# Kernel optimization log

Measured on AMD Instinct MI355X. Metric: run time of the kernel, lower is better.

## Reference

```python
import jax, jax.numpy as jnp
import numpy as np

N, B, T, F_IN, H1, H2 = 69, 32, 1024, 8, 32, 16


def cal_adj_norm(adj):
    # adj_norm = D^-1/2 (A + I) D^-1/2
    n = adj.shape[0]
    adj_ = adj + jnp.eye(n, dtype=adj.dtype)
    d = jnp.sum(adj_, axis=1)
    d_is = d ** -0.5
    return adj_ * d_is[:, None] * d_is[None, :]


def setup_inputs() -> dict:
    key = jax.random.key(0)
    k1, k2, k3, k4 = jax.random.split(key, 4)
    x = jax.random.normal(k1, (N, B, T, F_IN), dtype=jnp.float32)
    a = jax.random.uniform(k2, (N, N), dtype=jnp.float32)
    adj = ((a + a.T) > 1.4).astype(jnp.float32)
    W1 = jax.random.normal(k3, (F_IN, H1), dtype=jnp.float32)
    W2 = jax.random.normal(k4, (H1, H2), dtype=jnp.float32)
    return {"x": x, "adj": adj, "W1": W1, "W2": W2}


def reference(x, adj, W1, W2):
    adj_n = cal_adj_norm(adj)                      # [N, N]
    xb = jnp.transpose(x, (1, 2, 0, 3))            # [B, T, N, F_in]
    # layer 1: relu( adj_n @ x @ W1 ), batched over (B, T)
    h = jax.nn.relu(jnp.einsum('nm,btmf->btnf', adj_n, xb) @ W1)   # [B, T, N, H1]
    # layer 2: sigmoid( adj_n @ h @ W2 )
    out = jax.nn.sigmoid(jnp.einsum('nm,btmf->btnf', adj_n, h) @ W2)  # [B, T, N, H2]
    return out
```

## Files before the change

### kernel.cpp

```cpp
#include <hip/hip_runtime.h>
#include <math.h>

#define N_NODES 69
#define MP      80
#define KP      96
#define BT_TOTAL 32768
#define F_IN    8
#define H1      32
#define H2      16

#define TBT     8
#define BLOCK   256

#define ZPITCH  136
#define HBPITCH 40
#define RSTRIDE 72
#define RROWS   576

typedef __attribute__((ext_vector_type(8))) short bf16x8;
typedef __attribute__((ext_vector_type(4))) float f32x4;

__device__ __forceinline__ unsigned short f2bf(float f) {
    unsigned u = __float_as_uint(f);
    return (unsigned short)((u + 0x7FFFu + ((u >> 16) & 1u)) >> 16);
}
__device__ __forceinline__ float bf2f(unsigned short h) {
    return __uint_as_float(((unsigned)h) << 16);
}

__global__ void setup_kernel(const float* __restrict__ adj,
                             const float* __restrict__ W1,
                             const float* __restrict__ W2,
                             unsigned short* __restrict__ adjh,
                             unsigned short* __restrict__ adjl,
                             unsigned short* __restrict__ W1p,
                             unsigned short* __restrict__ W2p)
{
    __shared__ float dinv[N_NODES];
    const int tid = threadIdx.x;
    if (tid < N_NODES) {
        float s = 1.0f;
        for (int j = 0; j < N_NODES; ++j) s += adj[tid * N_NODES + j];
        dinv[tid] = rsqrtf(s);
    }
    __syncthreads();
    for (int idx = tid; idx < MP * KP; idx += BLOCK) {
        const int n = idx / KP, m = idx % KP;
        float v = 0.0f;
        if (n < N_NODES && m < N_NODES) {
            float a = adj[n * N_NODES + m] + (n == m ? 1.0f : 0.0f);
            v = a * dinv[n] * dinv[m];
        }
        unsigned short h = f2bf(v);
        adjh[idx] = h;
        adjl[idx] = f2bf(v - bf2f(h));
    }
    for (int i = tid; i < 2 * 64 * F_IN; i += BLOCK) {
        const int nt = i >> 9;
        const int ln = (i >> 3) & 63;
        const int j  = i & 7;
        const int q = ln >> 4, l = ln & 15;
        float v = (q == 0) ? W1[j * H1 + nt * 16 + l] : 0.0f;
        W1p[i] = f2bf(v);
    }
    for (int i = tid; i < 64 * F_IN; i += BLOCK) {
        const int ln = i >> 3, j = i & 7;
        const int q = ln >> 4, l = ln & 15;
        W2p[i] = f2bf(W2[(q * 8 + j) * H2 + l]);
    }
}

__global__ __launch_bounds__(BLOCK, 4) void gcn_kernel(
    const float* __restrict__ x,
    const unsigned short* __restrict__ adjh,
    const unsigned short* __restrict__ adjl,
    const unsigned short* __restrict__ W1p,
    const unsigned short* __restrict__ W2p,
    float* __restrict__ out)
{
    __shared__ unsigned short U_s[KP * ZPITCH];
    __shared__ unsigned short Y1_s[RROWS * F_IN];
    __shared__ unsigned short Hb_s[4][16 * HBPITCH];

    const int tid  = threadIdx.x;
    const int lane = tid & 63;
    const int wv   = tid >> 6;
    const int quad = lane >> 4;
    const int l16  = lane & 15;
    const int bt0  = blockIdx.x * TBT;

    for (int i = tid; i < 27 * 64; i += BLOCK) {
        const int row = N_NODES + (i >> 6), w = i & 63;
        ((unsigned*)U_s)[row * 68 + w] = 0u;
    }

    const int btg = bt0 + wv * 2 + (l16 >> 3);
    const int fl  = l16 & 7;

    f32x4 acc[5] = {};
#pragma unroll
    for (int kt = 0; kt < 3; ++kt) {
        union AF { unsigned u[4]; bf16x8 v; } ah, al;
#pragma unroll
        for (int p = 0; p < 4; ++p) {
            const int m0 = kt * 32 + quad * 8 + 2 * p;
            const int m1 = m0 + 1;
            float x0 = 0.0f, x1 = 0.0f;
            if (kt < 2) {
                x0 = x[(size_t)m0 * 262144 + btg * 8 + fl];
                x1 = x[(size_t)m1 * 262144 + btg * 8 + fl];
            } else {
                if (m0 < N_NODES) x0 = x[(size_t)m0 * 262144 + btg * 8 + fl];
                if (m1 < N_NODES) x1 = x[(size_t)m1 * 262144 + btg * 8 + fl];
            }
            const unsigned short h0 = f2bf(x0), h1 = f2bf(x1);
            ah.u[p] = (unsigned)h0 | ((unsigned)h1 << 16);
            const unsigned short g0 = f2bf(x0 - bf2f(h0));
            const unsigned short g1 = f2bf(x1 - bf2f(h1));
            al.u[p] = (unsigned)g0 | ((unsigned)g1 << 16);
        }
#pragma unroll
        for (int nt = 0; nt < 5; ++nt) {
            const int boff = (nt * 16 + l16) * KP + kt * 32 + quad * 8;
            const bf16x8 bh = *(const bf16x8*)(adjh + boff);
            const bf16x8 bl = *(const bf16x8*)(adjl + boff);
            acc[nt] = __builtin_amdgcn_mfma_f32_16x16x32_bf16(ah.v, bh, acc[nt], 0, 0, 0);
            acc[nt] = __builtin_amdgcn_mfma_f32_16x16x32_bf16(ah.v, bl, acc[nt], 0, 0, 0);
            acc[nt] = __builtin_amdgcn_mfma_f32_16x16x32_bf16(al.v, bh, acc[nt], 0, 0, 0);
        }
    }

    {
        const int btc = wv * 2 + (quad >> 1);
        const int fcb = (quad & 1) * 4;
#pragma unroll
        for (int nt = 0; nt < 5; ++nt) {
            const int n = nt * 16 + l16;
            if (n < RSTRIDE) {
#pragma unroll
                for (int reg = 0; reg < 4; ++reg)
                    Y1_s[(btc * RSTRIDE + n) * F_IN + fcb + reg] = f2bf(acc[nt][reg]);
            }
        }
    }

    const bf16x8 w1f0 = *(const bf16x8*)&W1p[lane * 8];
    const bf16x8 w1f1 = *(const bf16x8*)&W1p[(64 + lane) * 8];
    const bf16x8 w2f  = *(const bf16x8*)&W2p[lane * 8];

    unsigned short* Hb = Hb_s[wv];
#pragma unroll
    for (int mt2 = 0; mt2 < 9; ++mt2) {
        const int rb = wv * 144 + mt2 * 16;

        bf16x8 af = {0, 0, 0, 0, 0, 0, 0, 0};
        if (quad == 0)
            af = *(const bf16x8*)&Y1_s[(rb + l16) * F_IN];

        f32x4 h0 = {0.f, 0.f, 0.f, 0.f};
        f32x4 h1 = {0.f, 0.f, 0.f, 0.f};
        h0 = __builtin_amdgcn_mfma_f32_16x16x32_bf16(af, w1f0, h0, 0, 0, 0);
        h1 = __builtin_amdgcn_mfma_f32_16x16x32_bf16(af, w1f1, h1, 0, 0, 0);

#pragma unroll
        for (int reg = 0; reg < 4; ++reg) {
            const int row = quad * 4 + reg;
            Hb[row * HBPITCH + l16]      = f2bf(fmaxf(h0[reg], 0.f));
            Hb[row * HBPITCH + 16 + l16] = f2bf(fmaxf(h1[reg], 0.f));
        }
        const bf16x8 a2 = *(const bf16x8*)&Hb[l16 * HBPITCH + quad * 8];

        f32x4 zk = {0.f, 0.f, 0.f, 0.f};
        zk = __builtin_amdgcn_mfma_f32_16x16x32_bf16(a2, w2f, zk, 0, 0, 0);

#pragma unroll
        for (int reg = 0; reg < 4; ++reg) {
            const int r  = rb + quad * 4 + reg;
            const int bt = r / RSTRIDE;
            const int n  = r - bt * RSTRIDE;
            if (n < N_NODES)
                U_s[n * ZPITCH + bt * 16 + l16] = f2bf(zk[reg]);
        }
    }
    __syncthreads();

#pragma unroll
    for (int c = 0; c < 2; ++c) {
        const int ct3  = wv * 2 + c;
        const int col3 = ct3 * 16 + l16;
        bf16x8 bz[3];
#pragma unroll
        for (int kt = 0; kt < 3; ++kt) {
            const int k0 = kt * 32 + quad * 8;
#pragma unroll
            for (int j = 0; j < 8; ++j)
                bz[kt][j] = (short)U_s[(k0 + j) * ZPITCH + col3];
        }
#pragma unroll
        for (int mt = 0; mt < 5; ++mt) {
            f32x4 acc3 = {0.f, 0.f, 0.f, 0.f};
#pragma unroll
            for (int kt = 0; kt < 3; ++kt) {
                const bf16x8 ah =
                    *(const bf16x8*)(adjh + (mt * 16 + l16) * KP + kt * 32 + quad * 8);
                acc3 = __builtin_amdgcn_mfma_f32_16x16x32_bf16(ah, bz[kt], acc3, 0, 0, 0);
            }
#pragma unroll
            for (int reg = 0; reg < 4; ++reg) {
                const int n = mt * 16 + quad * 4 + reg;
                if (n < N_NODES) {
                    const float v = 1.0f / (1.0f + __expf(-acc3[reg]));
                    out[((size_t)(bt0 + ct3) * N_NODES + n) * H2 + l16] = v;
                }
            }
        }
    }
}

extern "C" void kernel_launch(void* const* d_in, const int* in_sizes, int n_in,
                              void* d_out, int out_size, void* d_ws, size_t ws_size,
                              hipStream_t stream) {
    const float* x   = (const float*)d_in[0];
    const float* adj = (const float*)d_in[1];
    const float* W1  = (const float*)d_in[2];
    const float* W2  = (const float*)d_in[3];
    float* out = (float*)d_out;

    unsigned short* adjh = (unsigned short*)d_ws;
    unsigned short* adjl = adjh + MP * KP;
    unsigned short* W1p  = adjl + MP * KP;
    unsigned short* W2p  = W1p + 2 * 64 * F_IN;

    setup_kernel<<<1, BLOCK, 0, stream>>>(adj, W1, W2, adjh, adjl, W1p, W2p);
    gcn_kernel<<<BT_TOTAL / TBT, BLOCK, 0, stream>>>(x, adjh, adjl, W1p, W2p, out);
}
```

Before: 264.6 us.

## Keep layer-1 aggregate in registers and transpose Z layout for vector LDS access

Drops the Y1 shared-memory round trip. The layer-1 aggregate accumulators are packed straight into MFMA A-fragments and multiplied against W1 fragments built in registers, with a split on quad halves. Z is now stored transposed (bt-major, node columns), so the final adjacency matmul can load B fragments with 16-byte vector LDS reads instead of scalar gathers, and adjacency fragments are shared across two column tiles. W1/W2 packing moves from the setup kernel into each block's global loads. Launch bounds rise to 5 blocks per CU because shared memory is smaller. The cost is more MFMAs on padded inputs and redundant per-block weight conversion.

```diff
diff --git a/kernel.cpp b/kernel.cpp
--- a/kernel.cpp
+++ b/kernel.cpp
@@ -12,13 +12,17 @@
 #define TBT     8
 #define BLOCK   256
 
-#define ZPITCH  136
+#define ZPITCH3 104
 #define HBPITCH 40
-#define RSTRIDE 72
-#define RROWS   576
 
 typedef __attribute__((ext_vector_type(8))) short bf16x8;
 typedef __attribute__((ext_vector_type(4))) float f32x4;
+typedef __attribute__((ext_vector_type(2), aligned(8)))  unsigned u32x2;
+typedef __attribute__((ext_vector_type(4), aligned(16))) unsigned u32x4;
+
+typedef bf16x8 __attribute__((may_alias)) bf16x8_a;
+typedef u32x2  __attribute__((may_alias)) u32x2_a;
+typedef u32x4  __attribute__((may_alias)) u32x4_a;
 
 __device__ __forceinline__ unsigned short f2bf(float f) {
     unsigned u = __float_as_uint(f);
@@ -29,12 +33,8 @@
 }
 
 __global__ void setup_kernel(const float* __restrict__ adj,
-                             const float* __restrict__ W1,
-                             const float* __restrict__ W2,
                              unsigned short* __restrict__ adjh,
-                             unsigned short* __restrict__ adjl,
-                             unsigned short* __restrict__ W1p,
-                             unsigned short* __restrict__ W2p)
+                             unsigned short* __restrict__ adjl)
 {
     __shared__ float dinv[N_NODES];
     const int tid = threadIdx.x;
@@ -55,31 +55,17 @@
         adjh[idx] = h;
         adjl[idx] = f2bf(v - bf2f(h));
     }
-    for (int i = tid; i < 2 * 64 * F_IN; i += BLOCK) {
-        const int nt = i >> 9;
-        const int ln = (i >> 3) & 63;
-        const int j  = i & 7;
-        const int q = ln >> 4, l = ln & 15;
-        float v = (q == 0) ? W1[j * H1 + nt * 16 + l] : 0.0f;
-        W1p[i] = f2bf(v);
-    }
-    for (int i = tid; i < 64 * F_IN; i += BLOCK) {
-        const int ln = i >> 3, j = i & 7;
-        const int q = ln >> 4, l = ln & 15;
-        W2p[i] = f2bf(W2[(q * 8 + j) * H2 + l]);
-    }
-}
-
-__global__ __launch_bounds__(BLOCK, 4) void gcn_kernel(
+}
+
+__global__ __launch_bounds__(BLOCK, 5) void gcn_kernel(
     const float* __restrict__ x,
     const unsigned short* __restrict__ adjh,
     const unsigned short* __restrict__ adjl,
-    const unsigned short* __restrict__ W1p,
-    const unsigned short* __restrict__ W2p,
+    const float* __restrict__ W1g,
+    const float* __restrict__ W2g,
     float* __restrict__ out)
 {
-    __shared__ unsigned short U_s[KP * ZPITCH];
-    __shared__ unsigned short Y1_s[RROWS * F_IN];
+    __shared__ unsigned short Zt[128 * ZPITCH3];
     __shared__ unsigned short Hb_s[4][16 * HBPITCH];
 
     const int tid  = threadIdx.x;
@@ -89,9 +75,10 @@
     const int l16  = lane & 15;
     const int bt0  = blockIdx.x * TBT;
 
-    for (int i = tid; i < 27 * 64; i += BLOCK) {
-        const int row = N_NODES + (i >> 6), w = i & 63;
-        ((unsigned*)U_s)[row * 68 + w] = 0u;
+    {
+        const int row = wv * 32 + (lane >> 1);
+        const int col = 80 + (lane & 1) * 8;
+        *(u32x4_a*)&Zt[row * ZPITCH3 + col] = (u32x4){0u, 0u, 0u, 0u};
     }
 
     const int btg = bt0 + wv * 2 + (l16 >> 3);
@@ -122,95 +109,98 @@
 #pragma unroll
         for (int nt = 0; nt < 5; ++nt) {
             const int boff = (nt * 16 + l16) * KP + kt * 32 + quad * 8;
-            const bf16x8 bh = *(const bf16x8*)(adjh + boff);
-            const bf16x8 bl = *(const bf16x8*)(adjl + boff);
+            const bf16x8 bh = *(const bf16x8_a*)(adjh + boff);
+            const bf16x8 bl = *(const bf16x8_a*)(adjl + boff);
             acc[nt] = __builtin_amdgcn_mfma_f32_16x16x32_bf16(ah.v, bh, acc[nt], 0, 0, 0);
             acc[nt] = __builtin_amdgcn_mfma_f32_16x16x32_bf16(ah.v, bl, acc[nt], 0, 0, 0);
             acc[nt] = __builtin_amdgcn_mfma_f32_16x16x32_bf16(al.v, bh, acc[nt], 0, 0, 0);
         }
     }
 
+    bf16x8 w1f[2][2] = {};
     {
-        const int btc = wv * 2 + (quad >> 1);
-        const int fcb = (quad & 1) * 4;
-#pragma unroll
-        for (int nt = 0; nt < 5; ++nt) {
-            const int n = nt * 16 + l16;
-            if (n < RSTRIDE) {
-#pragma unroll
-                for (int reg = 0; reg < 4; ++reg)
-                    Y1_s[(btc * RSTRIDE + n) * F_IN + fcb + reg] = f2bf(acc[nt][reg]);
+        const int fb0 = quad * 4;
+        const int fb1 = (quad - 2) * 4;
+#pragma unroll
+        for (int ht = 0; ht < 2; ++ht) {
+#pragma unroll
+            for (int j = 0; j < 4; ++j) {
+                const float a0 = (quad < 2)  ? W1g[(fb0 + j) * H1 + ht * 16 + l16] : 0.0f;
+                const float a1 = (quad >= 2) ? W1g[(fb1 + j) * H1 + ht * 16 + l16] : 0.0f;
+                w1f[0][ht][j] = (short)f2bf(a0);
+                w1f[1][ht][j] = (short)f2bf(a1);
             }
         }
     }
-
-    const bf16x8 w1f0 = *(const bf16x8*)&W1p[lane * 8];
-    const bf16x8 w1f1 = *(const bf16x8*)&W1p[(64 + lane) * 8];
-    const bf16x8 w2f  = *(const bf16x8*)&W2p[lane * 8];
+    bf16x8 w2f;
+#pragma unroll
+    for (int j = 0; j < 8; ++j)
+        w2f[j] = (short)f2bf(W2g[(quad * 8 + j) * H2 + l16]);
 
     unsigned short* Hb = Hb_s[wv];
-#pragma unroll
-    for (int mt2 = 0; mt2 < 9; ++mt2) {
-        const int rb = wv * 144 + mt2 * 16;
-
-        bf16x8 af = {0, 0, 0, 0, 0, 0, 0, 0};
-        if (quad == 0)
-            af = *(const bf16x8*)&Y1_s[(rb + l16) * F_IN];
-
-        f32x4 h0 = {0.f, 0.f, 0.f, 0.f};
-        f32x4 h1 = {0.f, 0.f, 0.f, 0.f};
-        h0 = __builtin_amdgcn_mfma_f32_16x16x32_bf16(af, w1f0, h0, 0, 0, 0);
-        h1 = __builtin_amdgcn_mfma_f32_16x16x32_bf16(af, w1f1, h1, 0, 0, 0);
-
+
+    auto do_bt = [&](const f32x4& h0, const f32x4& h1, int btl, int nt) {
 #pragma unroll
         for (int reg = 0; reg < 4; ++reg) {
             const int row = quad * 4 + reg;
             Hb[row * HBPITCH + l16]      = f2bf(fmaxf(h0[reg], 0.f));
             Hb[row * HBPITCH + 16 + l16] = f2bf(fmaxf(h1[reg], 0.f));
         }
-        const bf16x8 a2 = *(const bf16x8*)&Hb[l16 * HBPITCH + quad * 8];
-
+        const bf16x8 a2 = *(const bf16x8_a*)&Hb[l16 * HBPITCH + quad * 8];
         f32x4 zk = {0.f, 0.f, 0.f, 0.f};
         zk = __builtin_amdgcn_mfma_f32_16x16x32_bf16(a2, w2f, zk, 0, 0, 0);
-
-#pragma unroll
-        for (int reg = 0; reg < 4; ++reg) {
-            const int r  = rb + quad * 4 + reg;
-            const int bt = r / RSTRIDE;
-            const int n  = r - bt * RSTRIDE;
-            if (n < N_NODES)
-                U_s[n * ZPITCH + bt * 16 + l16] = f2bf(zk[reg]);
-        }
-    }
+        const unsigned z0 = (unsigned)f2bf(zk[0]) | ((unsigned)f2bf(zk[1]) << 16);
+        const unsigned z1 = (unsigned)f2bf(zk[2]) | ((unsigned)f2bf(zk[3]) << 16);
+        *(u32x2_a*)&Zt[(btl * 16 + l16) * ZPITCH3 + nt * 16 + quad * 4] = (u32x2){z0, z1};
+    };
+
+#pragma unroll
+    for (int nt = 0; nt < 5; ++nt) {
+        const unsigned d0 = (unsigned)f2bf(acc[nt][0]) | ((unsigned)f2bf(acc[nt][1]) << 16);
+        const unsigned d1 = (unsigned)f2bf(acc[nt][2]) | ((unsigned)f2bf(acc[nt][3]) << 16);
+        union AF { unsigned u[4]; bf16x8 v; } af;
+        af.u[0] = d0; af.u[1] = d1; af.u[2] = d0; af.u[3] = d1;
+
+        const f32x4 zz = {0.f, 0.f, 0.f, 0.f};
+        f32x4 hL0 = __builtin_amdgcn_mfma_f32_16x16x32_bf16(af.v, w1f[0][0], zz, 0, 0, 0);
+        f32x4 hL1 = __builtin_amdgcn_mfma_f32_16x16x32_bf16(af.v, w1f[0][1], zz, 0, 0, 0);
+        f32x4 hH0 = __builtin_amdgcn_mfma_f32_16x16x32_bf16(af.v, w1f[1][0], zz, 0, 0, 0);
+        f32x4 hH1 = __builtin_amdgcn_mfma_f32_16x16x32_bf16(af.v, w1f[1][1], zz, 0, 0, 0);
+
+        do_bt(hL0, hL1, wv * 2 + 0, nt);
+        do_bt(hH0, hH1, wv * 2 + 1, nt);
+    }
+
     __syncthreads();
 
-#pragma unroll
-    for (int c = 0; c < 2; ++c) {
-        const int ct3  = wv * 2 + c;
-        const int col3 = ct3 * 16 + l16;
-        bf16x8 bz[3];
-#pragma unroll
-        for (int kt = 0; kt < 3; ++kt) {
-            const int k0 = kt * 32 + quad * 8;
-#pragma unroll
-            for (int j = 0; j < 8; ++j)
-                bz[kt][j] = (short)U_s[(k0 + j) * ZPITCH + col3];
-        }
-#pragma unroll
-        for (int mt = 0; mt < 5; ++mt) {
-            f32x4 acc3 = {0.f, 0.f, 0.f, 0.f};
-#pragma unroll
-            for (int kt = 0; kt < 3; ++kt) {
-                const bf16x8 ah =
-                    *(const bf16x8*)(adjh + (mt * 16 + l16) * KP + kt * 32 + quad * 8);
-                acc3 = __builtin_amdgcn_mfma_f32_16x16x32_bf16(ah, bz[kt], acc3, 0, 0, 0);
-            }
+    bf16x8 bz[2][3];
+#pragma unroll
+    for (int c = 0; c < 2; ++c)
+#pragma unroll
+        for (int kt = 0; kt < 3; ++kt)
+            bz[c][kt] = *(const bf16x8_a*)
+                &Zt[((wv * 2 + c) * 16 + l16) * ZPITCH3 + kt * 32 + quad * 8];
+
+#pragma unroll
+    for (int mt = 0; mt < 5; ++mt) {
+        bf16x8 am[3];
+#pragma unroll
+        for (int kt = 0; kt < 3; ++kt)
+            am[kt] = *(const bf16x8_a*)&adjh[(mt * 16 + l16) * KP + kt * 32 + quad * 8];
+#pragma unroll
+        for (int c = 0; c < 2; ++c) {
+            f32x4 a3 = {0.f, 0.f, 0.f, 0.f};
+#pragma unroll
+            for (int kt = 0; kt < 3; ++kt)
+                a3 = __builtin_amdgcn_mfma_f32_16x16x32_bf16(am[kt], bz[c][kt], a3, 0, 0, 0);
+            const int ct3 = wv * 2 + c;
+            float* outc = out + ((size_t)(bt0 + ct3) * N_NODES) * H2 + l16;
 #pragma unroll
             for (int reg = 0; reg < 4; ++reg) {
                 const int n = mt * 16 + quad * 4 + reg;
                 if (n < N_NODES) {
-                    const float v = 1.0f / (1.0f + __expf(-acc3[reg]));
-                    out[((size_t)(bt0 + ct3) * N_NODES + n) * H2 + l16] = v;
+                    const float v = 1.0f / (1.0f + __expf(-a3[reg]));
+                    outc[n * H2] = v;
                 }
             }
         }
@@ -228,9 +218,7 @@
 
     unsigned short* adjh = (unsigned short*)d_ws;
     unsigned short* adjl = adjh + MP * KP;
-    unsigned short* W1p  = adjl + MP * KP;
-    unsigned short* W2p  = W1p + 2 * 64 * F_IN;
-
-    setup_kernel<<<1, BLOCK, 0, stream>>>(adj, W1, W2, adjh, adjl, W1p, W2p);
-    gcn_kernel<<<BT_TOTAL / TBT, BLOCK, 0, stream>>>(x, adjh, adjl, W1p, W2p, out);
-}
+
+    setup_kernel<<<1, BLOCK, 0, stream>>>(adj, adjh, adjl);
+    gcn_kernel<<<BT_TOTAL / TBT, BLOCK, 0, stream>>>(x, adjh, adjl, W1, W2, out);
+}
```

After: 267.4 us. About the same (+1.1%).
